# Performance work log

Hardware: AMD Instinct MI355X
Metric: run time of the kernel (lower is better)

The kernel has to match this reference:

```python
import jax, jax.numpy as jnp
import numpy as np

SEQ_LEN = 8
NUM_HEADS = 8
LN_EPS = 1e-5
GN_EPS = 64e-5  # GroupNorm eps = head_dim * 1e-5 (RWKV7 convention, head_dim=64)


def layer_norm(x, w, b):
    mu = x.mean(-1, keepdims=True)
    var = ((x - mu) ** 2).mean(-1, keepdims=True)
    return (x - mu) / jnp.sqrt(var + LN_EPS) * w + b


def token_shift(x):
    # delta = shift(x) - x; shift prepends one zero token along time
    return jnp.pad(x, ((0, 0), (1, 0), (0, 0)))[:, :-1] - x


def group_norm(x, w, b, H):
    B, T, C = x.shape
    xh = x.reshape(B, T, H, C // H)
    mu = xh.mean(-1, keepdims=True)
    var = ((xh - mu) ** 2).mean(-1, keepdims=True)
    return ((xh - mu) / jnp.sqrt(var + GN_EPS)).reshape(B, T, C) * w + b


def rwkv7_scan(r, w, k, v, a, b, H):
    # Generalized delta-rule recurrence (RWKV7):
    #   S_t = S_{t-1} * diag(exp(-exp(w_t))) + (S_{t-1} a_t) b_t^T + v_t k_t^T
    #   o_t = S_t r_t
    B, T, C = r.shape
    N = C // H

    def tm(x):  # [B,T,C] -> [T,B,H,N] (time-major for scan)
        return x.reshape(B, T, H, N).transpose(1, 0, 2, 3)

    decay = jnp.exp(-jnp.exp(tm(w)))
    rs, ks, vs, as_, bs = tm(r), tm(k), tm(v), tm(a), tm(b)

    def step(S, inp):
        rt, dt, kt, vt, at, bt = inp  # each [B,H,N]
        sa = jnp.einsum('bhij,bhj->bhi', S, at)
        S = (S * dt[:, :, None, :]
             + sa[..., None] * bt[:, :, None, :]
             + vt[..., None] * kt[:, :, None, :])
        return S, jnp.einsum('bhij,bhj->bhi', S, rt)

    S0 = jnp.zeros((B, H, N, N), r.dtype)
    _, out = jax.lax.scan(step, S0, (rs, decay, ks, vs, as_, bs))
    return out.transpose(1, 0, 2, 3).reshape(B, T, C)


def _forward(image_tensor, pos_emb, xm, w0, w1, w2, a0, a1, a2, v0, v1, v2,
             g1, g2, kkp, kap, rkp, Wr, Wk, Wv, Wo, lnx_w, lnx_b,
             ln1_w, ln1_b, ln2_w, ln2_b, fxk, Wkey, Wval, lnf_w, lnf_b):
    EB, C, ih, iw = image_tensor.shape
    B = EB // SEQ_LEN
    H = NUM_HEADS
    x = image_tensor.transpose(0, 2, 3, 1).reshape(EB, ih * iw, C)
    x = (x + pos_emb).reshape(B, SEQ_LEN * ih * iw, C)  # [B, T, C]
    L = Wr.shape[0]
    v_first = None
    for l in range(L):
        # ---- time mix (RWKV7 attention) ----
        h = layer_norm(x, ln1_w[l], ln1_b[l])
        Bh, T, _ = h.shape
        dx = token_shift(h)
        xr, xw, xk, xv, xa, xg = [h + dx * xm[l, i] for i in range(6)]
        r = xr @ Wr[l]
        w = -jax.nn.softplus(-(w0[l] + jnp.tanh(xw @ w1[l]) @ w2[l])) - 0.5
        k = xk @ Wk[l]
        v = xv @ Wv[l]
        if v_first is None:
            v_first = v
        else:
            v = v + (v_first - v) * jax.nn.sigmoid(v0[l] + (xv @ v1[l]) @ v2[l])
        a = jax.nn.sigmoid(a0[l] + (xa @ a1[l]) @ a2[l])  # in-context lr
        g = jax.nn.sigmoid(xg @ g1[l]) @ g2[l]
        kk = (k * kkp[l]).reshape(Bh, T, H, -1)
        kk = kk / jnp.maximum(jnp.linalg.norm(kk, axis=-1, keepdims=True), 1e-12)
        kk = kk.reshape(Bh, T, C)
        k = k * (1.0 + (a - 1.0) * kap[l])
        o = rwkv7_scan(r, w, k, v, -kk, kk * a, H)
        o = group_norm(o, lnx_w[l], lnx_b[l], H)
        r4, k4, v4 = (t.reshape(Bh, T, H, -1) for t in (r, k, v))
        o = o + ((r4 * k4 * rkp[l]).sum(-1, keepdims=True) * v4).reshape(Bh, T, C)
        x = x + (o * g) @ Wo[l]
        # ---- channel mix (squared-ReLU FFN) ----
        h = layer_norm(x, ln2_w[l], ln2_b[l])
        kf = h + token_shift(h) * fxk[l]
        x = x + jnp.square(jax.nn.relu(kf @ Wkey[l])) @ Wval[l]
    x = layer_norm(x, lnf_w, lnf_b)
    return x.reshape(EB, ih, iw, C).transpose(0, 3, 1, 2)


def setup_inputs() -> dict:
    key = jax.random.key(0)
    ks = jax.random.split(key, 24)
    L, C, H = 8, 512, 8
    DW, DA, DV, DG, FF = 64, 64, 32, 128, 2048
    EB, IV, IW = 32, 8, 16
    FS = IV * IW

    def n(k, shape, s=0.02):
        return jax.random.normal(k, shape, jnp.float32) * s

    return dict(
        image_tensor=jax.random.normal(ks[0], (EB, C, IV, IW), jnp.float32),
        pos_emb=n(ks[1], (1, FS, C)),
        xm=jax.random.uniform(ks[2], (L, 6, C), jnp.float32),
        w0=n(ks[3], (L, C), 0.5) - 0.5,
        w1=n(ks[4], (L, C, DW), 0.02), w2=n(ks[5], (L, DW, C), 0.1),
        a0=jnp.zeros((L, C), jnp.float32),
        a1=n(ks[6], (L, C, DA)), a2=n(ks[7], (L, DA, C), 0.1),
        v0=jnp.ones((L, C), jnp.float32),
        v1=n(ks[8], (L, C, DV)), v2=n(ks[9], (L, DV, C), 0.1),
        g1=n(ks[10], (L, C, DG)), g2=n(ks[11], (L, DG, C), 0.1),
        kkp=jnp.full((L, C), 0.85, jnp.float32),
        kap=jnp.ones((L, C), jnp.float32),
        rkp=n(ks[12], (L, H, C // H), 0.3),
        Wr=n(ks[13], (L, C, C)), Wk=n(ks[14], (L, C, C)),
        Wv=n(ks[15], (L, C, C)), Wo=n(ks[16], (L, C, C)),
        lnx_w=jnp.ones((L, C), jnp.float32), lnx_b=jnp.zeros((L, C), jnp.float32),
        ln1_w=jnp.ones((L, C), jnp.float32), ln1_b=jnp.zeros((L, C), jnp.float32),
        ln2_w=jnp.ones((L, C), jnp.float32), ln2_b=jnp.zeros((L, C), jnp.float32),
        fxk=jax.random.uniform(ks[17], (L, C), jnp.float32),
        Wkey=n(ks[18], (L, C, FF)), Wval=n(ks[19], (L, FF, C)),
        lnf_w=jnp.ones((C,), jnp.float32), lnf_b=jnp.zeros((C,), jnp.float32),
    )


def reference(image_tensor, pos_emb, xm, w0, w1, w2, a0, a1, a2, v0, v1, v2,
              g1, g2, kkp, kap, rkp, Wr, Wk, Wv, Wo, lnx_w, lnx_b,
              ln1_w, ln1_b, ln2_w, ln2_b, fxk, Wkey, Wval, lnf_w, lnf_b):
    return _forward(image_tensor, pos_emb, xm, w0, w1, w2, a0, a1, a2, v0, v1,
                    v2, g1, g2, kkp, kap, rkp, Wr, Wk, Wv, Wo, lnx_w, lnx_b,
                    ln1_w, ln1_b, ln2_w, ln2_b, fxk, Wkey, Wval, lnf_w, lnf_b)
```

## Files before the change

### kernel.cpp

```cpp
#include <hip/hip_runtime.h>
#include <hip/hip_bf16.h>
#include <math.h>


#define NTOK 4096
#define CDIM 512
#define TT   1024
#define LC   64
#define NCH  16
#define TB   8

#define BM 128
#define BN 128
#define BK 32

enum { EPI_NONE=0, EPI_TANH, EPI_SIG, EPI_DECAY, EPI_SIGB, EPI_VMIX, EPI_RELU2, EPI_ADD };

typedef short bf16x8 __attribute__((ext_vector_type(8)));
typedef float f32x4 __attribute__((ext_vector_type(4)));
typedef unsigned short ushort_t;

__device__ __forceinline__ float wsum64(float v) {
#pragma unroll
  for (int s = 1; s < 64; s <<= 1) v += __shfl_xor(v, s);
  return v;
}
__device__ __forceinline__ float gsum8(float v) {
  v += __shfl_xor(v, 1); v += __shfl_xor(v, 2); v += __shfl_xor(v, 4);
  return v;
}
__device__ __forceinline__ float sigm(float z) { return 1.f / (1.f + expf(-z)); }
__device__ __forceinline__ ushort_t f2bf(float x) {
  return __builtin_bit_cast(unsigned short, __float2bfloat16(x));
}
__device__ __forceinline__ void glds16(const void* g, void* l) {
  __builtin_amdgcn_global_load_lds(
      (const __attribute__((address_space(1))) void*)g,
      (__attribute__((address_space(3))) void*)l, 16, 0, 0);
}

struct Seg {
  const ushort_t* A; const ushort_t* B; void* C;
  const float* bias; const float* e1;
  int N; int K; int epi; int obf;
};
struct Segs4 { Seg s[4]; };

__global__ __launch_bounds__(256) void ggemm_k(Segs4 segs) {
  const Seg sg = segs.s[blockIdx.z];
  if (sg.epi < 0) return;
  __shared__ ushort_t As[2][BM * BK];
  __shared__ ushort_t Bs[2][BN * BK];
  const ushort_t* __restrict__ A = sg.A;
  const ushort_t* __restrict__ B = sg.B;
  const int N = sg.N, K = sg.K;
  const int tid = threadIdx.x;
  const int wave = tid >> 6, lane = tid & 63;
  const int m0 = blockIdx.x * BM, n0 = blockIdx.y * BN;
  const int wm = (wave >> 1) << 6, wn = (wave & 1) << 6;

  f32x4 zero = {0.f, 0.f, 0.f, 0.f};
  f32x4 acc[4][4];
#pragma unroll
  for (int i = 0; i < 4; ++i)
#pragma unroll
    for (int j = 0; j < 4; ++j) acc[i][j] = zero;

  const int c0 = wave << 1;
  const int srow0 = c0 * 16 + (lane >> 2);
  const int srow1 = srow0 + 16;
  const int soff0 = (((lane & 3) ^ (srow0 & 3)) << 3);
  const int soff1 = (((lane & 3) ^ (srow1 & 3)) << 3);
  const ushort_t* ga0 = A + (size_t)(m0 + srow0) * K + soff0;
  const ushort_t* ga1 = A + (size_t)(m0 + srow1) * K + soff1;
  const ushort_t* gb0 = B + (size_t)(n0 + srow0) * K + soff0;
  const ushort_t* gb1 = B + (size_t)(n0 + srow1) * K + soff1;

#define STAGE(bf_, k0_)                                \
  {                                                    \
    glds16(ga0 + (k0_), &As[bf_][(c0) * 512]);         \
    glds16(ga1 + (k0_), &As[bf_][(c0 + 1) * 512]);     \
    glds16(gb0 + (k0_), &Bs[bf_][(c0) * 512]);         \
    glds16(gb1 + (k0_), &Bs[bf_][(c0 + 1) * 512]);     \
  }

  const int rA = wm + (lane & 15);
  const int rB = wn + (lane & 15);
  const int kb = (((lane >> 4) ^ (lane & 3)) << 3);

#define COMPUTE(bf_)                                                          \
  {                                                                           \
    bf16x8 av[4], bvv[4];                                                     \
    _Pragma("unroll") for (int f = 0; f < 4; ++f) {                           \
      av[f]  = *(const bf16x8*)(&As[bf_][(rA + f * 16) * 32 + kb]);           \
      bvv[f] = *(const bf16x8*)(&Bs[bf_][(rB + f * 16) * 32 + kb]);           \
    }                                                                         \
    _Pragma("unroll") for (int i = 0; i < 4; ++i)                             \
      _Pragma("unroll") for (int j = 0; j < 4; ++j)                           \
        acc[i][j] = __builtin_amdgcn_mfma_f32_16x16x32_bf16(av[i], bvv[j],    \
                                                            acc[i][j], 0, 0, 0); \
  }

  STAGE(0, 0);
  __syncthreads();
  int buf = 0;
  for (int k0 = BK; k0 < K; k0 += BK) {
    STAGE(buf ^ 1, k0);
    COMPUTE(buf);
    __syncthreads();
    buf ^= 1;
  }
  COMPUTE(buf);
#undef STAGE
#undef COMPUTE

  void* Cout = sg.C;
  const float* bias = sg.bias;
  const float* e1 = sg.e1;
  const int em = m0 + wm + ((lane >> 4) << 2);
  const int en = n0 + wn + (lane & 15);

#define EPI_STORE(EPI_, OBF_)                                                 \
  { _Pragma("unroll") for (int fi = 0; fi < 4; ++fi) {                        \
      _Pragma("unroll") for (int fj = 0; fj < 4; ++fj) {                      \
        const int gn = en + fj * 16;                                          \
        if (gn < N) {                                                         \
          _Pragma("unroll") for (int rr = 0; rr < 4; ++rr) {                  \
            const int gm = em + fi * 16 + rr;                                 \
            const size_t idx = (size_t)gm * N + gn;                           \
            const float y = acc[fi][fj][rr];                                  \
            float outv;                                                       \
            if (EPI_ == EPI_NONE) { outv = y; }                               \
            else if (EPI_ == EPI_TANH) { outv = tanhf(y); }                   \
            else if (EPI_ == EPI_SIG) { outv = sigm(y); }                     \
            else if (EPI_ == EPI_DECAY) {                                     \
              const float z = bias[gn] + y;                                   \
              const float w = -log1pf(expf(-z)) - 0.5f;                       \
              outv = expf(-expf(w));                                          \
            } else if (EPI_ == EPI_SIGB) { outv = sigm(bias[gn] + y); }       \
            else if (EPI_ == EPI_VMIX) {                                      \
              const float vr = ((float*)Cout)[idx];                           \
              outv = vr + (e1[idx] - vr) * sigm(bias[gn] + y);                \
            } else if (EPI_ == EPI_RELU2) {                                   \
              const float t = fmaxf(y, 0.f); outv = t * t;                    \
            } else { outv = ((float*)Cout)[idx] + y; }                        \
            if (OBF_) ((ushort_t*)Cout)[idx] = f2bf(outv);                    \
            else      ((float*)Cout)[idx] = outv;                             \
          }                                                                   \
        }                                                                     \
      } } }

  switch (sg.epi) {
    case EPI_NONE:  if (sg.obf) EPI_STORE(EPI_NONE, 1) else EPI_STORE(EPI_NONE, 0); break;
    case EPI_TANH:  EPI_STORE(EPI_TANH, 1); break;
    case EPI_SIG:   EPI_STORE(EPI_SIG, 1); break;
    case EPI_DECAY: EPI_STORE(EPI_DECAY, 0); break;
    case EPI_SIGB:  EPI_STORE(EPI_SIGB, 0); break;
    case EPI_VMIX:  EPI_STORE(EPI_VMIX, 0); break;
    case EPI_RELU2: EPI_STORE(EPI_RELU2, 1); break;
    case EPI_ADD:   EPI_STORE(EPI_ADD, 0); break;
  }
#undef EPI_STORE
}

__global__ __launch_bounds__(256) void wprep_k(
    const float* __restrict__ in, ushort_t* __restrict__ out,
    int K, int N, int Npad)
{
  __shared__ float t[32][33];
  const int l = blockIdx.z;
  const int n0 = blockIdx.x * 32, k0 = blockIdx.y * 32;
  const int tx = threadIdx.x & 31, ty = threadIdx.x >> 5;
  const float* src = in + (size_t)l * K * N;
  ushort_t* dst = out + (size_t)l * Npad * K;
#pragma unroll
  for (int i = 0; i < 32; i += 8) {
    const int k = k0 + ty + i, n = n0 + tx;
    t[ty + i][tx] = (n < N) ? src[(size_t)k * N + n] : 0.f;
  }
  __syncthreads();
#pragma unroll
  for (int i = 0; i < 32; i += 8) {
    const int n = n0 + ty + i, k = k0 + tx;
    dst[(size_t)n * K + k] = f2bf(t[tx][ty + i]);
  }
}

__global__ __launch_bounds__(256) void lnmix6_k(
    const float* __restrict__ x, const float* __restrict__ w,
    const float* __restrict__ b, const float* __restrict__ xml,
    ushort_t* __restrict__ xr, ushort_t* __restrict__ xw,
    ushort_t* __restrict__ xk, ushort_t* __restrict__ xv,
    ushort_t* __restrict__ xa, ushort_t* __restrict__ xg)
{
  const int m = blockIdx.x * 4 + (threadIdx.x >> 6);
  const int lane = threadIdx.x & 63;
  const int c0 = lane << 3;
  const size_t idx = (size_t)m * CDIM + c0;
  const bool first = ((m & (TT - 1)) == 0);
  float v[8], p[8];
  *(float4*)&v[0] = *(const float4*)&x[idx];
  *(float4*)&v[4] = *(const float4*)&x[idx + 4];
  if (first) {
#pragma unroll
    for (int j = 0; j < 8; ++j) p[j] = 0.f;
  } else {
    *(float4*)&p[0] = *(const float4*)&x[idx - CDIM];
    *(float4*)&p[4] = *(const float4*)&x[idx - CDIM + 4];
  }
  float s = 0.f, sp = 0.f;
#pragma unroll
  for (int j = 0; j < 8; ++j) { s += v[j]; sp += p[j]; }
  s = wsum64(s); sp = wsum64(sp);
  const float mu = s * (1.f / 512.f), mup = sp * (1.f / 512.f);
  float q = 0.f, qp = 0.f;
#pragma unroll
  for (int j = 0; j < 8; ++j) {
    const float d1 = v[j] - mu, d2 = p[j] - mup;
    q += d1 * d1; qp += d2 * d2;
  }
  q = wsum64(q); qp = wsum64(qp);
  const float is = rsqrtf(q * (1.f / 512.f) + 1e-5f);
  const float isp = rsqrtf(qp * (1.f / 512.f) + 1e-5f);
  float wc[8], bc[8];
  *(float4*)&wc[0] = *(const float4*)&w[c0]; *(float4*)&wc[4] = *(const float4*)&w[c0 + 4];
  *(float4*)&bc[0] = *(const float4*)&b[c0]; *(float4*)&bc[4] = *(const float4*)&b[c0 + 4];
  float hv[8], dx[8];
#pragma unroll
  for (int j = 0; j < 8; ++j) {
    hv[j] = (v[j] - mu) * is * wc[j] + bc[j];
    const float hp = first ? 0.f : (p[j] - mup) * isp * wc[j] + bc[j];
    dx[j] = hp - hv[j];
  }
  ushort_t* outs[6] = {xr, xw, xk, xv, xa, xg};
#pragma unroll
  for (int o = 0; o < 6; ++o) {
    float mc[8];
    *(float4*)&mc[0] = *(const float4*)&xml[o * CDIM + c0];
    *(float4*)&mc[4] = *(const float4*)&xml[o * CDIM + c0 + 4];
    bf16x8 pk;
#pragma unroll
    for (int j = 0; j < 8; ++j) pk[j] = (short)f2bf(fmaf(dx[j], mc[j], hv[j]));
    *(bf16x8*)&outs[o][idx] = pk;
  }
}

__global__ __launch_bounds__(256) void lnmix1_k(
    const float* __restrict__ x, const float* __restrict__ w,
    const float* __restrict__ b, const float* __restrict__ coef,
    ushort_t* __restrict__ kf)
{
  const int m = blockIdx.x * 4 + (threadIdx.x >> 6);
  const int lane = threadIdx.x & 63;
  const int c0 = lane << 3;
  const size_t idx = (size_t)m * CDIM + c0;
  const bool first = ((m & (TT - 1)) == 0);
  float v[8], p[8];
  *(float4*)&v[0] = *(const float4*)&x[idx];
  *(float4*)&v[4] = *(const float4*)&x[idx + 4];
  if (first) {
#pragma unroll
    for (int j = 0; j < 8; ++j) p[j] = 0.f;
  } else {
    *(float4*)&p[0] = *(const float4*)&x[idx - CDIM];
    *(float4*)&p[4] = *(const float4*)&x[idx - CDIM + 4];
  }
  float s = 0.f, sp = 0.f;
#pragma unroll
  for (int j = 0; j < 8; ++j) { s += v[j]; sp += p[j]; }
  s = wsum64(s); sp = wsum64(sp);
  const float mu = s * (1.f / 512.f), mup = sp * (1.f / 512.f);
  float q = 0.f, qp = 0.f;
#pragma unroll
  for (int j = 0; j < 8; ++j) {
    const float d1 = v[j] - mu, d2 = p[j] - mup;
    q += d1 * d1; qp += d2 * d2;
  }
  q = wsum64(q); qp = wsum64(qp);
  const float is = rsqrtf(q * (1.f / 512.f) + 1e-5f);
  const float isp = rsqrtf(qp * (1.f / 512.f) + 1e-5f);
  bf16x8 pk;
#pragma unroll
  for (int j = 0; j < 8; ++j) {
    const float wc = w[c0 + j], bc = b[c0 + j];
    const float hv = (v[j] - mu) * is * wc + bc;
    const float hp = first ? 0.f : (p[j] - mup) * isp * wc + bc;
    pk[j] = (short)f2bf(fmaf(hp - hv, coef[c0 + j], hv));
  }
  *(bf16x8*)&kf[idx] = pk;
}

__global__ __launch_bounds__(256) void prep_k(
    float* __restrict__ k, const float* __restrict__ a,
    const float* __restrict__ kkp, const float* __restrict__ kap,
    float* __restrict__ aa, float* __restrict__ bb)
{
  const int m = blockIdx.x * 4 + (threadIdx.x >> 6);
  const int lane = threadIdx.x & 63;
  const int c0 = lane << 3;
  const size_t idx = (size_t)m * CDIM + c0;
  float kv[8], av[8], kp[8], ka[8];
  *(float4*)&kv[0] = *(const float4*)&k[idx];     *(float4*)&kv[4] = *(const float4*)&k[idx + 4];
  *(float4*)&av[0] = *(const float4*)&a[idx];     *(float4*)&av[4] = *(const float4*)&a[idx + 4];
  *(float4*)&kp[0] = *(const float4*)&kkp[c0];    *(float4*)&kp[4] = *(const float4*)&kkp[c0 + 4];
  *(float4*)&ka[0] = *(const float4*)&kap[c0];    *(float4*)&ka[4] = *(const float4*)&kap[c0 + 4];
  float kk[8], ss = 0.f;
#pragma unroll
  for (int j = 0; j < 8; ++j) { kk[j] = kv[j] * kp[j]; ss += kk[j] * kk[j]; }
  ss = gsum8(ss);
  const float rden = 1.f / fmaxf(sqrtf(ss), 1e-12f);
  float oaa[8], obb[8], okk[8];
#pragma unroll
  for (int j = 0; j < 8; ++j) {
    const float kkn = kk[j] * rden;
    oaa[j] = -kkn;
    obb[j] = kkn * av[j];
    okk[j] = kv[j] * (1.f + (av[j] - 1.f) * ka[j]);
  }
  *(float4*)&aa[idx] = *(float4*)&oaa[0]; *(float4*)&aa[idx + 4] = *(float4*)&oaa[4];
  *(float4*)&bb[idx] = *(float4*)&obb[0]; *(float4*)&bb[idx + 4] = *(float4*)&obb[4];
  *(float4*)&k[idx]  = *(float4*)&okk[0]; *(float4*)&k[idx + 4]  = *(float4*)&okk[4];
}

__global__ __launch_bounds__(256) void post_k(
    const float* __restrict__ o, const float* __restrict__ r,
    const float* __restrict__ k, const float* __restrict__ v,
    const float* __restrict__ g, const float* __restrict__ gw,
    const float* __restrict__ gb, const float* __restrict__ rkp,
    ushort_t* __restrict__ og)
{
  const int m = blockIdx.x * 4 + (threadIdx.x >> 6);
  const int lane = threadIdx.x & 63;
  const int c0 = lane << 3;
  const size_t idx = (size_t)m * CDIM + c0;
  float ov[8], rv[8], kv[8], vv[8], gv[8], rp[8];
  *(float4*)&ov[0] = *(const float4*)&o[idx];   *(float4*)&ov[4] = *(const float4*)&o[idx + 4];
  *(float4*)&rv[0] = *(const float4*)&r[idx];   *(float4*)&rv[4] = *(const float4*)&r[idx + 4];
  *(float4*)&kv[0] = *(const float4*)&k[idx];   *(float4*)&kv[4] = *(const float4*)&k[idx + 4];
  *(float4*)&vv[0] = *(const float4*)&v[idx];   *(float4*)&vv[4] = *(const float4*)&v[idx + 4];
  *(float4*)&gv[0] = *(const float4*)&g[idx];   *(float4*)&gv[4] = *(const float4*)&g[idx + 4];
  *(float4*)&rp[0] = *(const float4*)&rkp[c0];  *(float4*)&rp[4] = *(const float4*)&rkp[c0 + 4];
  float s = 0.f, dot = 0.f;
#pragma unroll
  for (int j = 0; j < 8; ++j) { s += ov[j]; dot += rv[j] * kv[j] * rp[j]; }
  s = gsum8(s); dot = gsum8(dot);
  const float mu = s * (1.f / 64.f);
  float q = 0.f;
#pragma unroll
  for (int j = 0; j < 8; ++j) { const float d = ov[j] - mu; q += d * d; }
  q = gsum8(q);
  const float is = rsqrtf(q * (1.f / 64.f) + 64e-5f);
  bf16x8 pk;
#pragma unroll
  for (int j = 0; j < 8; ++j) {
    const float gn = (ov[j] - mu) * is * gw[c0 + j] + gb[c0 + j];
    pk[j] = (short)f2bf((gn + dot * vv[j]) * gv[j]);
  }
  *(bf16x8*)&og[idx] = pk;
}

__global__ __launch_bounds__(512) void ln_final_k(
    const float* __restrict__ x, const float* __restrict__ w,
    const float* __restrict__ b, float* __restrict__ out)
{
  const int m = blockIdx.x, c = threadIdx.x;
  const size_t idx = (size_t)m * CDIM + c;
  const float v = x[idx];
  __shared__ float red[8], red2[8];
  float s = wsum64(v);
  if ((c & 63) == 0) red[c >> 6] = s;
  __syncthreads();
  float tot = 0.f;
#pragma unroll
  for (int u = 0; u < 8; ++u) tot += red[u];
  const float mu = tot * (1.f / 512.f);
  const float dv = v - mu;
  float s2 = wsum64(dv * dv);
  if ((c & 63) == 0) red2[c >> 6] = s2;
  __syncthreads();
  float vt = 0.f;
#pragma unroll
  for (int u = 0; u < 8; ++u) vt += red2[u];
  const float y = dv * rsqrtf(vt * (1.f / 512.f) + 1e-5f) * w[c] + b[c];
  const int bidx = m >> 10, t = m & 1023;
  const int p = t & 127, eb = bidx * 8 + (t >> 7);
  out[((size_t)eb * CDIM + c) * 128 + p] = y;
}

__global__ __launch_bounds__(512) void build_x_k(
    const float* __restrict__ img, const float* __restrict__ pos,
    float* __restrict__ x)
{
  const int m = blockIdx.x, c = threadIdx.x;
  const int bidx = m >> 10, t = m & 1023;
  const int p = t & 127, eb = bidx * 8 + (t >> 7);
  x[(size_t)m * CDIM + c] =
      img[((size_t)eb * CDIM + c) * 128 + p] + pos[(size_t)p * CDIM + c];
}

__global__ __launch_bounds__(256) void scan1_k(
    const float* __restrict__ d, const float* __restrict__ k,
    const float* __restrict__ v, const float* __restrict__ aa,
    const float* __restrict__ bb,
    float* __restrict__ P, float* __restrict__ Q)
{
  const int ch = blockIdx.x, bh = blockIdx.y;
  const int b = bh >> 3, hh = bh & 7;
  const int tid = threadIdx.x;
  const int i = tid >> 2, j0 = (tid & 3) << 4;
  float S[16], Pr[16];
#pragma unroll
  for (int u = 0; u < 16; ++u) { S[u] = 0.f; Pr[u] = (j0 + u == i) ? 1.f : 0.f; }

  __shared__ float sbuf[2][5 * TB * 64];
  const size_t base = (size_t)b * TT * CDIM + (size_t)ch * LC * CDIM + hh * 64;
  const float* srcs[5] = {d, k, v, aa, bb};
  const int f0 = tid, f1 = tid + 256, f2 = tid + 512;
  const float* gp0 = srcs[f0 >> 7] + base + (size_t)((f0 >> 4) & 7) * CDIM + ((f0 & 15) << 2);
  const float* gp1 = srcs[f1 >> 7] + base + (size_t)((f1 >> 4) & 7) * CDIM + ((f1 & 15) << 2);
  const float* gp2 = (tid < 128)
      ? srcs[f2 >> 7] + base + (size_t)((f2 >> 4) & 7) * CDIM + ((f2 & 15) << 2)
      : srcs[0];

#define STAGE1(bf_, goff_)                                   \
  {                                                          \
    glds16(gp0 + (goff_), &sbuf[bf_][f0 << 2]);              \
    glds16(gp1 + (goff_), &sbuf[bf_][f1 << 2]);              \
    if (tid < 128) glds16(gp2 + (goff_), &sbuf[bf_][f2 << 2]); \
  }

  STAGE1(0, 0);
  __syncthreads();
  int buf = 0;
  for (int g = 0; g < LC / TB; ++g) {
    if (g + 1 < LC / TB) STAGE1(buf ^ 1, (size_t)(g + 1) * TB * CDIM);
    const float* sb0 = sbuf[buf];
#pragma unroll
    for (int tt = 0; tt < TB; ++tt) {
      const float* sd = sb0 + 0 * TB * 64 + tt * 64;
      const float* sk = sb0 + 1 * TB * 64 + tt * 64;
      const float* sv = sb0 + 2 * TB * 64 + tt * 64;
      const float* sa = sb0 + 3 * TB * 64 + tt * 64;
      const float* sbv = sb0 + 4 * TB * 64 + tt * 64;

      float ps = 0.f, pp = 0.f;
#pragma unroll
      for (int jj = 0; jj < 16; ++jj) {
        ps = fmaf(S[jj],  sa[j0 + jj], ps);
        pp = fmaf(Pr[jj], sa[j0 + jj], pp);
      }
      ps += __shfl_xor(ps, 1); ps += __shfl_xor(ps, 2);
      pp += __shfl_xor(pp, 1); pp += __shfl_xor(pp, 2);
      const float vi = sv[i];
#pragma unroll
      for (int jj = 0; jj < 16; ++jj) {
        S[jj]  = fmaf(S[jj],  sd[j0 + jj], fmaf(ps, sbv[j0 + jj], vi * sk[j0 + jj]));
        Pr[jj] = fmaf(Pr[jj], sd[j0 + jj], pp * sbv[j0 + jj]);
      }
    }
    __syncthreads();
    buf ^= 1;
  }
#undef STAGE1

  const size_t ob = ((size_t)(bh * NCH + ch)) * 4096 + (size_t)i * 64 + j0;
#pragma unroll
  for (int u = 0; u < 4; ++u) {
    *(float4*)&Q[ob + 4 * u] = make_float4(S[4*u], S[4*u+1], S[4*u+2], S[4*u+3]);
    *(float4*)&P[ob + 4 * u] = make_float4(Pr[4*u], Pr[4*u+1], Pr[4*u+2], Pr[4*u+3]);
  }
}

__global__ __launch_bounds__(512) void scan2_k(
    const float* __restrict__ P, const float* __restrict__ Q,
    float* __restrict__ Sst)
{
  const int tid = threadIdx.x;
  const int f0 = tid << 2;
  const int r0 = tid >> 4;
  const int c0 = (tid & 15) << 2;
  __shared__ float sP[4096];
  __shared__ float sS[4096];
  float4 S0 = {0.f, 0.f, 0.f, 0.f}, S1 = {0.f, 0.f, 0.f, 0.f};
  const size_t cbase = (size_t)blockIdx.x * NCH * 4096;
  float4 pf0 = *(const float4*)&P[cbase + f0];
  float4 pf1 = *(const float4*)&P[cbase + f0 + 2048];

  for (int c = 0; c < NCH; ++c) {
    const size_t cb = cbase + (size_t)c * 4096;
    *(float4*)&Sst[cb + f0] = S0;
    *(float4*)&Sst[cb + f0 + 2048] = S1;
    __syncthreads();
    *(float4*)&sP[f0] = pf0;  *(float4*)&sP[f0 + 2048] = pf1;
    *(float4*)&sS[f0] = S0;   *(float4*)&sS[f0 + 2048] = S1;
    __syncthreads();
    if (c + 1 < NCH) {
      pf0 = *(const float4*)&P[cb + 4096 + f0];
      pf1 = *(const float4*)&P[cb + 4096 + f0 + 2048];
    }
    const float4 q0 = *(const float4*)&Q[cb + f0];
    const float4 q1 = *(const float4*)&Q[cb + f0 + 2048];

    float a00 = 0.f, a01 = 0.f, a02 = 0.f, a03 = 0.f;
    float a10 = 0.f, a11 = 0.f, a12 = 0.f, a13 = 0.f;
    const float* sS0 = &sS[r0 * 64];
    const float* sS1 = &sS[(r0 + 32) * 64];
#pragma unroll
    for (int mm = 0; mm < 64; ++mm) {
      const float4 p4 = *(const float4*)&sP[mm * 64 + c0];
      const float u0 = sS0[mm], u1 = sS1[mm];
      a00 = fmaf(u0, p4.x, a00); a01 = fmaf(u0, p4.y, a01);
      a02 = fmaf(u0, p4.z, a02); a03 = fmaf(u0, p4.w, a03);
      a10 = fmaf(u1, p4.x, a10); a11 = fmaf(u1, p4.y, a11);
      a12 = fmaf(u1, p4.z, a12); a13 = fmaf(u1, p4.w, a13);
    }
    S0.x = a00 + q0.x; S0.y = a01 + q0.y; S0.z = a02 + q0.z; S0.w = a03 + q0.w;
    S1.x = a10 + q1.x; S1.y = a11 + q1.y; S1.z = a12 + q1.z; S1.w = a13 + q1.w;
  }
}

__global__ __launch_bounds__(256) void scan3_k(
    const float* __restrict__ r, const float* __restrict__ d,
    const float* __restrict__ k, const float* __restrict__ v,
    const float* __restrict__ aa, const float* __restrict__ bb,
    const float* __restrict__ Sst, float* __restrict__ o)
{
  const int ch = blockIdx.x, bh = blockIdx.y;
  const int b = bh >> 3, hh = bh & 7;
  const int tid = threadIdx.x;
  const int i = tid >> 2, q = tid & 3, j0 = q << 4;
  float S[16];
  const size_t sb_ = ((size_t)(bh * NCH + ch)) * 4096 + (size_t)i * 64 + j0;
#pragma unroll
  for (int u = 0; u < 4; ++u) {
    const float4 s4 = *(const float4*)&Sst[sb_ + 4 * u];
    S[4*u] = s4.x; S[4*u+1] = s4.y; S[4*u+2] = s4.z; S[4*u+3] = s4.w;
  }

  __shared__ float sbuf[2][6 * TB * 64];
  const size_t base = (size_t)b * TT * CDIM + (size_t)ch * LC * CDIM + hh * 64;
  const float* srcs[6] = {r, d, k, v, aa, bb};
  const int f0 = tid, f1 = tid + 256, f2 = tid + 512;
  const float* gp0 = srcs[f0 >> 7] + base + (size_t)((f0 >> 4) & 7) * CDIM + ((f0 & 15) << 2);
  const float* gp1 = srcs[f1 >> 7] + base + (size_t)((f1 >> 4) & 7) * CDIM + ((f1 & 15) << 2);
  const float* gp2 = srcs[f2 >> 7] + base + (size_t)((f2 >> 4) & 7) * CDIM + ((f2 & 15) << 2);

#define STAGE3(bf_, goff_)                          \
  {                                                 \
    glds16(gp0 + (goff_), &sbuf[bf_][f0 << 2]);     \
    glds16(gp1 + (goff_), &sbuf[bf_][f1 << 2]);     \
    glds16(gp2 + (goff_), &sbuf[bf_][f2 << 2]);     \
  }

  STAGE3(0, 0);
  __syncthreads();
  int buf = 0;
  for (int g = 0; g < LC / TB; ++g) {
    if (g + 1 < LC / TB) STAGE3(buf ^ 1, (size_t)(g + 1) * TB * CDIM);
    const float* sb0 = sbuf[buf];
    const size_t obase = base + (size_t)g * TB * CDIM;
#pragma unroll
    for (int tt = 0; tt < TB; ++tt) {
      const float* sr = sb0 + 0 * TB * 64 + tt * 64;
      const float* sd = sb0 + 1 * TB * 64 + tt * 64;
      const float* sk = sb0 + 2 * TB * 64 + tt * 64;
      const float* sv = sb0 + 3 * TB * 64 + tt * 64;
      const float* sa = sb0 + 4 * TB * 64 + tt * 64;
      const float* sbv = sb0 + 5 * TB * 64 + tt * 64;

      float ps = 0.f, ps1 = 0.f;
#pragma unroll
      for (int jj = 0; jj < 16; jj += 2) {
        ps  = fmaf(S[jj],     sa[j0 + jj],     ps);
        ps1 = fmaf(S[jj + 1], sa[j0 + jj + 1], ps1);
      }
      ps += ps1;
      ps += __shfl_xor(ps, 1); ps += __shfl_xor(ps, 2);
      const float vi = sv[i];

      float po = 0.f, po1 = 0.f;
#pragma unroll
      for (int jj = 0; jj < 16; jj += 2) {
        float s0 = fmaf(S[jj],     sd[j0 + jj],     fmaf(ps, sbv[j0 + jj],     vi * sk[j0 + jj]));
        float s1 = fmaf(S[jj + 1], sd[j0 + jj + 1], fmaf(ps, sbv[j0 + jj + 1], vi * sk[j0 + jj + 1]));
        S[jj] = s0; S[jj + 1] = s1;
        po  = fmaf(s0, sr[j0 + jj],     po);
        po1 = fmaf(s1, sr[j0 + jj + 1], po1);
      }
      po += po1;
      po += __shfl_xor(po, 1); po += __shfl_xor(po, 2);
      if (q == 0) o[obase + (size_t)tt * CDIM + i] = po;
    }
    __syncthreads();
    buf ^= 1;
  }
#undef STAGE3
}

extern "C" void kernel_launch(void* const* d_in, const int* in_sizes, int n_in,
                              void* d_out, int out_size, void* d_ws, size_t ws_size,
                              hipStream_t stream) {
  (void)in_sizes; (void)n_in; (void)out_size; (void)ws_size;
  const float* img  = (const float*)d_in[0];
  const float* pos  = (const float*)d_in[1];
  const float* xm   = (const float*)d_in[2];
  const float* w0   = (const float*)d_in[3];
  const float* w1   = (const float*)d_in[4];
  const float* w2   = (const float*)d_in[5];
  const float* a0   = (const float*)d_in[6];
  const float* a1   = (const float*)d_in[7];
  const float* a2   = (const float*)d_in[8];
  const float* v0   = (const float*)d_in[9];
  const float* v1   = (const float*)d_in[10];
  const float* v2   = (const float*)d_in[11];
  const float* g1   = (const float*)d_in[12];
  const float* g2   = (const float*)d_in[13];
  const float* kkp  = (const float*)d_in[14];
  const float* kap  = (const float*)d_in[15];
  const float* rkp  = (const float*)d_in[16];
  const float* Wr   = (const float*)d_in[17];
  const float* Wk   = (const float*)d_in[18];
  const float* Wv   = (const float*)d_in[19];
  const float* Wo   = (const float*)d_in[20];
  const float* lnxw = (const float*)d_in[21];
  const float* lnxb = (const float*)d_in[22];
  const float* ln1w = (const float*)d_in[23];
  const float* ln1b = (const float*)d_in[24];
  const float* ln2w = (const float*)d_in[25];
  const float* ln2b = (const float*)d_in[26];
  const float* fxk  = (const float*)d_in[27];
  const float* Wkey = (const float*)d_in[28];
  const float* Wval = (const float*)d_in[29];
  const float* lnfw = (const float*)d_in[30];
  const float* lnfb = (const float*)d_in[31];

  float* ws = (float*)d_ws;
  const size_t SZ = (size_t)NTOK * CDIM;
  float* x   = ws + 0 * SZ;
  float* r_  = ws + 2 * SZ;
  float* dec = ws + 3 * SZ;
  float* k_  = ws + 4 * SZ;
  float* v_  = ws + 5 * SZ;
  float* vf  = ws + 6 * SZ;
  float* a_  = ws + 7 * SZ;
  float* g_  = ws + 8 * SZ;
  float* aa  = ws + 9 * SZ;
  float* bb  = ws + 10 * SZ;
  float* o_  = ws + 11 * SZ;
  float* mixf = ws + 12 * SZ;
  ushort_t* xr = (ushort_t*)mixf;
  ushort_t* xw = xr + SZ;
  ushort_t* xk = xr + 2 * SZ;
  ushort_t* xv = xr + 3 * SZ;
  ushort_t* xa = xr + 4 * SZ;
  ushort_t* xg = xr + 5 * SZ;
  float* Pbuf = mixf;
  float* Qbuf = mixf + SZ;
  float* Sst  = mixf + 2 * SZ;
  ushort_t* tmpb = (ushort_t*)(ws + 15 * SZ);
  ushort_t* t0b = tmpb;
  ushort_t* t1b = tmpb + (size_t)NTOK * 64;
  ushort_t* t2b = tmpb + (size_t)NTOK * 128;
  ushort_t* t3b = tmpb + (size_t)NTOK * 160;
  ushort_t* tfb  = (ushort_t*)(ws + 15 * SZ + SZ / 2);
  ushort_t* ogb  = (ushort_t*)(ws + 17 * SZ + SZ / 2);
  ushort_t* wb   = (ushort_t*)(ws + 18 * SZ);

  const size_t oWr  = 0;
  const size_t oWk  = oWr  + (size_t)8 * 512 * 512;
  const size_t oWv  = oWk  + (size_t)8 * 512 * 512;
  const size_t oWo  = oWv  + (size_t)8 * 512 * 512;
  const size_t oW1  = oWo  + (size_t)8 * 512 * 512;
  const size_t oW2  = oW1  + (size_t)8 * 128 * 512;
  const size_t oA1  = oW2  + (size_t)8 * 512 * 64;
  const size_t oA2  = oA1  + (size_t)8 * 128 * 512;
  const size_t oV1  = oA2  + (size_t)8 * 512 * 64;
  const size_t oV2  = oV1  + (size_t)8 * 128 * 512;
  const size_t oG1  = oV2  + (size_t)8 * 512 * 32;
  const size_t oG2  = oG1  + (size_t)8 * 128 * 512;
  const size_t oKey = oG2  + (size_t)8 * 512 * 128;
  const size_t oVal = oKey + (size_t)8 * 2048 * 512;

#define WPREP(src, dst, K_, N_, NP_) \
  wprep_k<<<dim3((NP_) / 32, (K_) / 32, 8), 256, 0, stream>>>(src, dst, K_, N_, NP_)
  WPREP(Wr,   wb + oWr,  512, 512, 512);
  WPREP(Wk,   wb + oWk,  512, 512, 512);
  WPREP(Wv,   wb + oWv,  512, 512, 512);
  WPREP(Wo,   wb + oWo,  512, 512, 512);
  WPREP(w1,   wb + oW1,  512, 64,  128);
  WPREP(w2,   wb + oW2,  64,  512, 512);
  WPREP(a1,   wb + oA1,  512, 64,  128);
  WPREP(a2,   wb + oA2,  64,  512, 512);
  WPREP(v1,   wb + oV1,  512, 32,  128);
  WPREP(v2,   wb + oV2,  32,  512, 512);
  WPREP(g1,   wb + oG1,  512, 128, 128);
  WPREP(g2,   wb + oG2,  128, 512, 512);
  WPREP(Wkey, wb + oKey, 512, 2048, 2048);
  WPREP(Wval, wb + oVal, 2048, 512, 512);
#undef WPREP

  build_x_k<<<NTOK, 512, 0, stream>>>(img, pos, x);

  for (int l = 0; l < 8; ++l) {
    const size_t lc = (size_t)l * CDIM;
    const float* xml = xm + (size_t)l * 6 * CDIM;
    const ushort_t* bWr = wb + oWr + (size_t)l * 512 * 512;
    const ushort_t* bWk = wb + oWk + (size_t)l * 512 * 512;
    const ushort_t* bWv = wb + oWv + (size_t)l * 512 * 512;
    const ushort_t* bWo = wb + oWo + (size_t)l * 512 * 512;
    const ushort_t* bW1 = wb + oW1 + (size_t)l * 128 * 512;
    const ushort_t* bW2 = wb + oW2 + (size_t)l * 512 * 64;
    const ushort_t* bA1 = wb + oA1 + (size_t)l * 128 * 512;
    const ushort_t* bA2 = wb + oA2 + (size_t)l * 512 * 64;
    const ushort_t* bV1 = wb + oV1 + (size_t)l * 128 * 512;
    const ushort_t* bV2 = wb + oV2 + (size_t)l * 512 * 32;
    const ushort_t* bG1 = wb + oG1 + (size_t)l * 128 * 512;
    const ushort_t* bG2 = wb + oG2 + (size_t)l * 512 * 128;
    const ushort_t* bKy = wb + oKey + (size_t)l * 2048 * 512;
    const ushort_t* bVl = wb + oVal + (size_t)l * 512 * 2048;
    float* vdst = (l == 0) ? vf : v_;

    lnmix6_k<<<NTOK / 4, 256, 0, stream>>>(x, ln1w + lc, ln1b + lc, xml,
                                           xr, xw, xk, xv, xa, xg);
    Segs4 qkv;
    qkv.s[0] = {xr, bWr, r_,   0, 0, 512, 512, EPI_NONE, 0};
    qkv.s[1] = {xk, bWk, k_,   0, 0, 512, 512, EPI_NONE, 0};
    qkv.s[2] = {xv, bWv, vdst, 0, 0, 512, 512, EPI_NONE, 0};
    qkv.s[3] = {0, 0, 0, 0, 0, 0, 0, -1, 0};
    ggemm_k<<<dim3(NTOK / BM, 4, 3), 256, 0, stream>>>(qkv);

    Segs4 dn;
    dn.s[0] = {xw, bW1, t0b, 0, 0, 64,  512, EPI_TANH, 1};
    dn.s[1] = {xa, bA1, t1b, 0, 0, 64,  512, EPI_NONE, 1};
    dn.s[2] = {xv, bV1, t2b, 0, 0, 32,  512, EPI_NONE, 1};
    dn.s[3] = {xg, bG1, t3b, 0, 0, 128, 512, EPI_SIG,  1};
    ggemm_k<<<dim3(NTOK / BM, 1, 4), 256, 0, stream>>>(dn);

    Segs4 up;
    up.s[0] = {t0b, bW2, dec, w0 + lc, 0,  512, 64,  EPI_DECAY, 0};
    up.s[1] = {t1b, bA2, a_,  a0 + lc, 0,  512, 64,  EPI_SIGB,  0};
    up.s[2] = {t2b, bV2, v_,  v0 + lc, vf, 512, 32,  (l > 0) ? EPI_VMIX : -1, 0};
    up.s[3] = {t3b, bG2, g_,  0, 0,        512, 128, EPI_NONE,  0};
    ggemm_k<<<dim3(NTOK / BM, 4, 4), 256, 0, stream>>>(up);

    const float* vptr = (l == 0) ? vf : v_;
    prep_k<<<NTOK / 4, 256, 0, stream>>>(k_, a_, kkp + lc, kap + lc, aa, bb);
    scan1_k<<<dim3(NCH, 32), 256, 0, stream>>>(dec, k_, vptr, aa, bb, Pbuf, Qbuf);
    scan2_k<<<32, 512, 0, stream>>>(Pbuf, Qbuf, Sst);
    scan3_k<<<dim3(NCH, 32), 256, 0, stream>>>(r_, dec, k_, vptr, aa, bb, Sst, o_);
    post_k<<<NTOK / 4, 256, 0, stream>>>(o_, r_, k_, vptr, g_, lnxw + lc, lnxb + lc,
                                         rkp + lc, ogb);
    Segs4 wo;
    wo.s[0] = {ogb, bWo, x, 0, 0, 512, 512, EPI_ADD, 0};
    wo.s[1] = wo.s[2] = wo.s[3] = {0, 0, 0, 0, 0, 0, 0, -1, 0};
    ggemm_k<<<dim3(NTOK / BM, 4, 1), 256, 0, stream>>>(wo);

    lnmix1_k<<<NTOK / 4, 256, 0, stream>>>(x, ln2w + lc, ln2b + lc, fxk + lc, xr);
    Segs4 f1;
    f1.s[0] = {xr, bKy, tfb, 0, 0, 2048, 512, EPI_RELU2, 1};
    f1.s[1] = f1.s[2] = f1.s[3] = {0, 0, 0, 0, 0, 0, 0, -1, 0};
    ggemm_k<<<dim3(NTOK / BM, 16, 1), 256, 0, stream>>>(f1);
    Segs4 f2;
    f2.s[0] = {tfb, bVl, x, 0, 0, 512, 2048, EPI_ADD, 0};
    f2.s[1] = f2.s[2] = f2.s[3] = {0, 0, 0, 0, 0, 0, 0, -1, 0};
    ggemm_k<<<dim3(NTOK / BM, 4, 1), 256, 0, stream>>>(f2);
  }

  ln_final_k<<<NTOK, 512, 0, stream>>>(x, lnfw, lnfb, (float*)d_out);
}
```

Baseline: 2.719 ms.

## Template GEMM on N-tile, use 64-wide tiles and triple-buffered async loads

Turns the grouped GEMM kernel into a template on the N tile width, and every call site now launches it with BN=64, which doubles the block count so more of the GPU's compute units get work on these small GEMMs. The K loop moves from a double buffer with a full sync per step to a three-stage LDS ring, using explicit vmcnt waits plus raw barriers so loads for step k+2 overlap compute on step k. The trade-off is more A-tile reloads per output, less MFMA work per wave (4x2 fragments instead of 4x4) and more LDS per block. The hand-written waitcnt depends on the per-thread count of outstanding loads (LPW) being exact.

```diff
diff --git a/kernel.cpp b/kernel.cpp
--- a/kernel.cpp
+++ b/kernel.cpp
@@ -11,7 +11,6 @@
 #define TB   8
 
 #define BM 128
-#define BN 128
 #define BK 32
 
 enum { EPI_NONE=0, EPI_TANH, EPI_SIG, EPI_DECAY, EPI_SIGB, EPI_VMIX, EPI_RELU2, EPI_ADD };
@@ -46,43 +45,52 @@
 };
 struct Segs4 { Seg s[4]; };
 
+template<int BNt>
 __global__ __launch_bounds__(256) void ggemm_k(Segs4 segs) {
   const Seg sg = segs.s[blockIdx.z];
   if (sg.epi < 0) return;
-  __shared__ ushort_t As[2][BM * BK];
-  __shared__ ushort_t Bs[2][BN * BK];
+  constexpr int NCHK = 8 + BNt / 16;
+  constexpr int LPW  = NCHK / 4;
+  constexpr int WNF  = BNt / 32;
+  __shared__ ushort_t As[3][BM * BK];
+  __shared__ ushort_t Bs[3][BNt * BK];
   const ushort_t* __restrict__ A = sg.A;
   const ushort_t* __restrict__ B = sg.B;
   const int N = sg.N, K = sg.K;
   const int tid = threadIdx.x;
   const int wave = tid >> 6, lane = tid & 63;
-  const int m0 = blockIdx.x * BM, n0 = blockIdx.y * BN;
-  const int wm = (wave >> 1) << 6, wn = (wave & 1) << 6;
+  const int m0 = blockIdx.x * BM, n0 = blockIdx.y * BNt;
+  const int wm = (wave >> 1) << 6, wn = (wave & 1) * (BNt / 2);
 
   f32x4 zero = {0.f, 0.f, 0.f, 0.f};
-  f32x4 acc[4][4];
+  f32x4 acc[4][WNF];
 #pragma unroll
   for (int i = 0; i < 4; ++i)
 #pragma unroll
-    for (int j = 0; j < 4; ++j) acc[i][j] = zero;
-
-  const int c0 = wave << 1;
-  const int srow0 = c0 * 16 + (lane >> 2);
-  const int srow1 = srow0 + 16;
-  const int soff0 = (((lane & 3) ^ (srow0 & 3)) << 3);
-  const int soff1 = (((lane & 3) ^ (srow1 & 3)) << 3);
-  const ushort_t* ga0 = A + (size_t)(m0 + srow0) * K + soff0;
-  const ushort_t* ga1 = A + (size_t)(m0 + srow1) * K + soff1;
-  const ushort_t* gb0 = B + (size_t)(n0 + srow0) * K + soff0;
-  const ushort_t* gb1 = B + (size_t)(n0 + srow1) * K + soff1;
-
-#define STAGE(bf_, k0_)                                \
-  {                                                    \
-    glds16(ga0 + (k0_), &As[bf_][(c0) * 512]);         \
-    glds16(ga1 + (k0_), &As[bf_][(c0 + 1) * 512]);     \
-    glds16(gb0 + (k0_), &Bs[bf_][(c0) * 512]);         \
-    glds16(gb1 + (k0_), &Bs[bf_][(c0 + 1) * 512]);     \
-  }
+    for (int j = 0; j < WNF; ++j) acc[i][j] = zero;
+
+  const int crow = lane >> 2;
+  const int soff = (((lane & 3) ^ (crow & 3)) << 3);
+  const ushort_t* gptr[LPW];
+  ushort_t* lbase[LPW];
+  int lstr[LPW];
+#pragma unroll
+  for (int i = 0; i < LPW; ++i) {
+    const int c = wave + 4 * i;
+    if (c < 8) {
+      gptr[i] = A + (size_t)(m0 + c * 16 + crow) * K + soff;
+      lbase[i] = &As[0][c * 512 + lane * 8];
+      lstr[i] = BM * BK;
+    } else {
+      gptr[i] = B + (size_t)(n0 + (c - 8) * 16 + crow) * K + soff;
+      lbase[i] = &Bs[0][(c - 8) * 512 + lane * 8];
+      lstr[i] = BNt * BK;
+    }
+  }
+
+#define STAGE(bf_, k0_)                                        \
+  { _Pragma("unroll") for (int i = 0; i < LPW; ++i)            \
+      glds16(gptr[i] + (k0_), lbase[i] + (bf_) * lstr[i]); }
 
   const int rA = wm + (lane & 15);
   const int rB = wn + (lane & 15);
@@ -90,27 +98,34 @@
 
 #define COMPUTE(bf_)                                                          \
   {                                                                           \
-    bf16x8 av[4], bvv[4];                                                     \
-    _Pragma("unroll") for (int f = 0; f < 4; ++f) {                           \
-      av[f]  = *(const bf16x8*)(&As[bf_][(rA + f * 16) * 32 + kb]);           \
+    bf16x8 av[4], bvv[WNF];                                                   \
+    _Pragma("unroll") for (int f = 0; f < 4; ++f)                             \
+      av[f] = *(const bf16x8*)(&As[bf_][(rA + f * 16) * 32 + kb]);            \
+    _Pragma("unroll") for (int f = 0; f < WNF; ++f)                           \
       bvv[f] = *(const bf16x8*)(&Bs[bf_][(rB + f * 16) * 32 + kb]);           \
-    }                                                                         \
     _Pragma("unroll") for (int i = 0; i < 4; ++i)                             \
-      _Pragma("unroll") for (int j = 0; j < 4; ++j)                           \
+      _Pragma("unroll") for (int j = 0; j < WNF; ++j)                         \
         acc[i][j] = __builtin_amdgcn_mfma_f32_16x16x32_bf16(av[i], bvv[j],    \
                                                             acc[i][j], 0, 0, 0); \
   }
 
+  const int nk = K / BK;
   STAGE(0, 0);
-  __syncthreads();
-  int buf = 0;
-  for (int k0 = BK; k0 < K; k0 += BK) {
-    STAGE(buf ^ 1, k0);
-    COMPUTE(buf);
-    __syncthreads();
-    buf ^= 1;
-  }
-  COMPUTE(buf);
+  if (nk > 1) STAGE(1, BK);
+  int bc = 0, bs = 2;
+  for (int k = 0; k + 1 < nk; ++k) {
+    asm volatile("s_waitcnt vmcnt(%0)" :: "i"(LPW) : "memory");
+    __builtin_amdgcn_s_barrier();
+    if (k + 2 < nk) {
+      STAGE(bs, (k + 2) * BK);
+      bs = (bs == 2) ? 0 : bs + 1;
+    }
+    COMPUTE(bc);
+    bc = (bc == 2) ? 0 : bc + 1;
+  }
+  asm volatile("s_waitcnt vmcnt(0)" ::: "memory");
+  __builtin_amdgcn_s_barrier();
+  COMPUTE(bc);
 #undef STAGE
 #undef COMPUTE
 
@@ -122,7 +137,7 @@
 
 #define EPI_STORE(EPI_, OBF_)                                                 \
   { _Pragma("unroll") for (int fi = 0; fi < 4; ++fi) {                        \
-      _Pragma("unroll") for (int fj = 0; fj < 4; ++fj) {                      \
+      _Pragma("unroll") for (int fj = 0; fj < WNF; ++fj) {                    \
         const int gn = en + fj * 16;                                          \
         if (gn < N) {                                                         \
           _Pragma("unroll") for (int rr = 0; rr < 4; ++rr) {                  \
@@ -727,21 +742,21 @@
     qkv.s[1] = {xk, bWk, k_,   0, 0, 512, 512, EPI_NONE, 0};
     qkv.s[2] = {xv, bWv, vdst, 0, 0, 512, 512, EPI_NONE, 0};
     qkv.s[3] = {0, 0, 0, 0, 0, 0, 0, -1, 0};
-    ggemm_k<<<dim3(NTOK / BM, 4, 3), 256, 0, stream>>>(qkv);
+    ggemm_k<64><<<dim3(NTOK / BM, 8, 3), 256, 0, stream>>>(qkv);
 
     Segs4 dn;
     dn.s[0] = {xw, bW1, t0b, 0, 0, 64,  512, EPI_TANH, 1};
     dn.s[1] = {xa, bA1, t1b, 0, 0, 64,  512, EPI_NONE, 1};
     dn.s[2] = {xv, bV1, t2b, 0, 0, 32,  512, EPI_NONE, 1};
     dn.s[3] = {xg, bG1, t3b, 0, 0, 128, 512, EPI_SIG,  1};
-    ggemm_k<<<dim3(NTOK / BM, 1, 4), 256, 0, stream>>>(dn);
+    ggemm_k<64><<<dim3(NTOK / BM, 2, 4), 256, 0, stream>>>(dn);
 
     Segs4 up;
     up.s[0] = {t0b, bW2, dec, w0 + lc, 0,  512, 64,  EPI_DECAY, 0};
     up.s[1] = {t1b, bA2, a_,  a0 + lc, 0,  512, 64,  EPI_SIGB,  0};
     up.s[2] = {t2b, bV2, v_,  v0 + lc, vf, 512, 32,  (l > 0) ? EPI_VMIX : -1, 0};
     up.s[3] = {t3b, bG2, g_,  0, 0,        512, 128, EPI_NONE,  0};
-    ggemm_k<<<dim3(NTOK / BM, 4, 4), 256, 0, stream>>>(up);
+    ggemm_k<64><<<dim3(NTOK / BM, 8, 4), 256, 0, stream>>>(up);
 
     const float* vptr = (l == 0) ? vf : v_;
     prep_k<<<NTOK / 4, 256, 0, stream>>>(k_, a_, kkp + lc, kap + lc, aa, bb);
@@ -753,17 +768,17 @@
     Segs4 wo;
     wo.s[0] = {ogb, bWo, x, 0, 0, 512, 512, EPI_ADD, 0};
     wo.s[1] = wo.s[2] = wo.s[3] = {0, 0, 0, 0, 0, 0, 0, -1, 0};
-    ggemm_k<<<dim3(NTOK / BM, 4, 1), 256, 0, stream>>>(wo);
+    ggemm_k<64><<<dim3(NTOK / BM, 8, 1), 256, 0, stream>>>(wo);
 
     lnmix1_k<<<NTOK / 4, 256, 0, stream>>>(x, ln2w + lc, ln2b + lc, fxk + lc, xr);
     Segs4 f1;
     f1.s[0] = {xr, bKy, tfb, 0, 0, 2048, 512, EPI_RELU2, 1};
     f1.s[1] = f1.s[2] = f1.s[3] = {0, 0, 0, 0, 0, 0, 0, -1, 0};
-    ggemm_k<<<dim3(NTOK / BM, 16, 1), 256, 0, stream>>>(f1);
+    ggemm_k<64><<<dim3(NTOK / BM, 32, 1), 256, 0, stream>>>(f1);
     Segs4 f2;
     f2.s[0] = {tfb, bVl, x, 0, 0, 512, 2048, EPI_ADD, 0};
     f2.s[1] = f2.s[2] = f2.s[3] = {0, 0, 0, 0, 0, 0, 0, -1, 0};
-    ggemm_k<<<dim3(NTOK / BM, 4, 1), 256, 0, stream>>>(f2);
+    ggemm_k<64><<<dim3(NTOK / BM, 8, 1), 256, 0, stream>>>(f2);
   }
 
   ln_final_k<<<NTOK, 512, 0, stream>>>(x, lnfw, lnfb, (float*)d_out);
```

New measurement: 2.248 ms. 1.21x faster.
